# Kernel tuning notes

Hardware: AMD Instinct MI355X
Metric: run time of the kernel (lower is better)

The kernel has to match this reference:

```python
import jax, jax.numpy as jnp
import numpy as np

K, N, D, M, M_RF, N_RF = 512, 512, 16, 64, 16, 64


def cmul(a, b):
    # complex matmul with stacked real/imag in axis -3: a [...,2,m,k], b [...,2,k,n]
    ar, ai = a[..., 0, :, :], a[..., 1, :, :]
    br, bi = b[..., 0, :, :], b[..., 1, :, :]
    return jnp.stack([ar @ br - ai @ bi, ar @ bi + ai @ br], axis=-3)


def conjT(a):
    # complex conjugate transpose
    ar, ai = a[..., 0, :, :], a[..., 1, :, :]
    return jnp.stack([jnp.swapaxes(ar, -1, -2), -jnp.swapaxes(ai, -1, -2)], axis=-3)


def cinv(a):
    # inverse of complex matrix a=[2,n,n] via real 2n x 2n block matrix
    ar, ai = a[0], a[1]
    n = ar.shape[0]
    Mblk = jnp.block([[ar, -ai], [ai, ar]])
    Minv = jnp.linalg.inv(Mblk)
    return jnp.stack([Minv[:n, :n], Minv[n:, :n]], axis=0)


def setup_inputs() -> dict:
    key = jax.random.key(0)
    ks = jax.random.split(key, 8)
    s = 0.05  # keep accumulated products well-scaled
    H = s * jax.random.normal(ks[0], (K, 2, M, N), jnp.float32)
    U_RF = s * jax.random.normal(ks[1], (K, 2, M, M_RF), jnp.float32)
    U_BB = s * jax.random.normal(ks[2], (K, 2, M_RF, D), jnp.float32)
    W = s * jax.random.normal(ks[3], (K, 2, D, D), jnp.float32)
    V_RF = s * jax.random.normal(ks[4], (2, N, N_RF), jnp.float32)
    V_BB = s * jax.random.normal(ks[5], (K, 2, N_RF, D), jnp.float32)
    Y = s * jax.random.normal(ks[6], (K, 2, N, D), jnp.float32)
    rho = jnp.ones((1,), jnp.float32)  # forward arg, unused by the module
    rho_X_layer = jnp.asarray(6.0, jnp.float32)  # learned scalar
    mu = jnp.asarray(1.0, jnp.float32)           # learned scalar
    params4 = 0.001 * jax.random.normal(ks[7], (K, 2, N, D), jnp.float32)
    return dict(H=H, U_RF=U_RF, U_BB=U_BB, W=W, V_RF=V_RF, V_BB=V_BB, Y=Y,
                rho=rho, rho_X_layer=rho_X_layer, mu=mu, params4=params4)


def reference(H, U_RF, U_BB, W, V_RF, V_BB, Y, rho, rho_X_layer, mu, params4):
    # temp[k] = H[k]^H U_RF[k] U_BB[k] : [K,2,N,d]
    temp = cmul(cmul(conjT(H), U_RF), U_BB)
    TW = cmul(temp, W)  # [K,2,N,d]
    # A_rho = sum_k temp W temp^H + I/(2 rho) : [2,N,N]
    A_rho = cmul(TW, conjT(temp)).sum(axis=0)
    I = jnp.stack([jnp.eye(N, dtype=H.dtype), jnp.zeros((N, N), H.dtype)], axis=0)
    A_rho = A_rho + (1.0 / (2.0 * rho_X_layer)) * I
    # B_rho[k] = temp W + 0.5*(V_RF V_BB[k]/rho - Y[k]) : [K,2,N,d]
    B_rho = TW + 0.5 * ((1.0 / rho_X_layer) * cmul(V_RF, V_BB) - Y)
    A_inv = cinv(A_rho + mu * I)  # [2,N,N]
    X = cmul(A_inv, B_rho) + params4  # [K,2,N,d]
    return X
```

## Files before the change

kernel.cpp:

```cpp
#include <hip/hip_runtime.h>

#define KK 512
#define NN 512
#define DD 16
#define MM 64
#define MRF 16
#define NRF 64

typedef __attribute__((ext_vector_type(8))) short bf16x8;
typedef __attribute__((ext_vector_type(4))) float f32x4;
typedef __attribute__((ext_vector_type(8))) unsigned short u16x8;
typedef __attribute__((ext_vector_type(4))) unsigned short u16x4;

#define MFMA16 __builtin_amdgcn_mfma_f32_16x16x32_bf16

static __device__ __forceinline__ unsigned short f2bf(float x) {
    unsigned int u = __float_as_uint(x);
    u += 0x7fffu + ((u >> 16) & 1u);
    return (unsigned short)(u >> 16);
}
static __device__ __forceinline__ float bf2f(unsigned short b) {
    return __uint_as_float((unsigned int)b << 16);
}

__global__ __launch_bounds__(256) void vrfb_kernel(
    const float* __restrict__ V_RF, unsigned short* __restrict__ VRFb)
{
    const int idx = blockIdx.x*256 + threadIdx.x;
    const int n = idx >> 7, j = idx & 127;
    const int p = j >> 6, r = j & 63;
    VRFb[idx] = f2bf(V_RF[((size_t)p*NN + n)*NRF + r]);
}

__global__ __launch_bounds__(256) void small_kernel(
    const float* __restrict__ U_RF, const float* __restrict__ U_BB,
    const float* __restrict__ W, const float* __restrict__ V_BB,
    unsigned short* __restrict__ GT2, unsigned short* __restrict__ VBT2)
{
    const int k = blockIdx.x, t = threadIdx.x;
    __shared__ float sUR[2][MM][17];
    __shared__ float sUB[2][MRF][DD], sW[2][DD][DD];
    __shared__ float sVB[2][NRF][17];
    __shared__ float sG[2][MM][17], sGW[2][MM][17];

    const float* uf = U_RF + (size_t)k*2*MM*MRF;
    for (int i = t; i < 2*MM*MRF; i += 256) sUR[i>>10][(i>>4)&63][i&15] = uf[i];
    const float* ub = U_BB + (size_t)k*2*MRF*DD;
    for (int i = t; i < 2*MRF*DD; i += 256) sUB[i>>8][(i>>4)&15][i&15] = ub[i];
    const float* ww = W + (size_t)k*2*DD*DD;
    for (int i = t; i < 2*DD*DD; i += 256) sW[i>>8][(i>>4)&15][i&15] = ww[i];
    const float* vb = V_BB + (size_t)k*2*NRF*DD;
    for (int i = t; i < 2*NRF*DD; i += 256) sVB[i>>10][(i>>4)&63][i&15] = vb[i];
    __syncthreads();

    {
        const int m = t >> 2, dq = (t & 3) * 4;
        float gr[4] = {0,0,0,0}, gi[4] = {0,0,0,0};
#pragma unroll
        for (int r = 0; r < MRF; ++r) {
            const float ur = sUR[0][m][r], ui = sUR[1][m][r];
#pragma unroll
            for (int q = 0; q < 4; ++q) {
                const float br = sUB[0][r][dq+q], bi = sUB[1][r][dq+q];
                gr[q] += ur*br - ui*bi;
                gi[q] += ur*bi + ui*br;
            }
        }
#pragma unroll
        for (int q = 0; q < 4; ++q) { sG[0][m][dq+q] = gr[q]; sG[1][m][dq+q] = gi[q]; }
    }
    __syncthreads();

    {
        const int m = t >> 2, dq = (t & 3) * 4;
        float gwr[4] = {0,0,0,0}, gwi[4] = {0,0,0,0};
#pragma unroll
        for (int dp = 0; dp < DD; ++dp) {
            const float gr = sG[0][m][dp], gi = sG[1][m][dp];
#pragma unroll
            for (int q = 0; q < 4; ++q) {
                const float wr = sW[0][dp][dq+q], wi = sW[1][dp][dq+q];
                gwr[q] += gr*wr - gi*wi;
                gwi[q] += gr*wi + gi*wr;
            }
        }
#pragma unroll
        for (int q = 0; q < 4; ++q) { sGW[0][m][dq+q] = gwr[q]; sGW[1][m][dq+q] = gwi[q]; }
    }
    __syncthreads();

    {
        const int row = t >> 2, cq = t & 3;
        const int s = row >> 4, d = row & 15;
        const float (*P)[MM][17] = (s < 2) ? sG : sGW;
        const int im = s & 1;
        unsigned short* dst = GT2 + (((size_t)k*4 + s)*DD + d)*128;
#pragma unroll
        for (int cb = 0; cb < 4; ++cb) {
            u16x8 pk;
#pragma unroll
            for (int q = 0; q < 8; ++q) {
                const int c = cb*32 + cq*8 + q;
                const int m = c & 63, hi = c >> 6;
                float v;
                if (!im) v = hi ? P[1][m][d] : P[0][m][d];
                else     v = hi ? -P[0][m][d] : P[1][m][d];
                pk[q] = f2bf(v);
            }
            *reinterpret_cast<u16x8*>(dst + cb*32 + cq*8) = pk;
        }
    }
    {
        const int row = t >> 3, cq = t & 7;
        const int s = row >> 4, d = row & 15;
        unsigned short* dst = VBT2 + (((size_t)k*2 + s)*DD + d)*128;
#pragma unroll
        for (int cb = 0; cb < 2; ++cb) {
            u16x8 pk;
#pragma unroll
            for (int q = 0; q < 8; ++q) {
                const int c = cb*64 + cq*8 + q;
                const int r = c & 63, hi = c >> 6;
                float v;
                if (s == 0) v = hi ? -sVB[1][r][d] : sVB[0][r][d];
                else        v = hi ?  sVB[0][r][d] : sVB[1][r][d];
                pk[q] = f2bf(v);
            }
            *reinterpret_cast<u16x8*>(dst + cb*64 + cq*8) = pk;
        }
    }
}

__global__ __launch_bounds__(256) void prep_main(
    const float* __restrict__ H, const unsigned short* __restrict__ GT2,
    const unsigned short* __restrict__ VBT2, const unsigned short* __restrict__ VRFb,
    const float* __restrict__ Y, const float* __restrict__ rhoX,
    unsigned short* __restrict__ tempb, unsigned short* __restrict__ TWb,
    unsigned short* __restrict__ Bb)
{
    const int k  = blockIdx.x;
    const int nq = blockIdx.y;
    const int w = threadIdx.x >> 6, lane = threadIdx.x & 63;
    const int c = lane & 15, kg = lane >> 4;
    const float irx = 1.f / rhoX[0];

    const int nA = nq*128 + w*32 + c;
    const int nB = nA + 16;
    const float* Hk = H + (size_t)k*128*NN;

    f32x4 acc[12];
#pragma unroll
    for (int q = 0; q < 12; ++q) acc[q] = (f32x4)0.f;

#pragma unroll
    for (int ks = 0; ks < 4; ++ks) {
        const int slot0 = ks*32 + kg*8;
        const unsigned short* gbase = GT2 + ((size_t)k*4*DD + c)*128 + slot0;
        const bf16x8 g0 = *reinterpret_cast<const bf16x8*>(gbase);
        const bf16x8 g1 = *reinterpret_cast<const bf16x8*>(gbase + (size_t)DD*128);
        const bf16x8 g2 = *reinterpret_cast<const bf16x8*>(gbase + (size_t)2*DD*128);
        const bf16x8 g3 = *reinterpret_cast<const bf16x8*>(gbase + (size_t)3*DD*128);
        const unsigned short* vbase = VBT2 + ((size_t)k*2*DD + c)*128 + slot0;
        const bf16x8 v0 = *reinterpret_cast<const bf16x8*>(vbase);
        const bf16x8 v1 = *reinterpret_cast<const bf16x8*>(vbase + (size_t)DD*128);

        float hA[8], hB[8];
#pragma unroll
        for (int e = 0; e < 8; ++e) {
            hA[e] = Hk[(size_t)(slot0 + e)*NN + nA];
            hB[e] = Hk[(size_t)(slot0 + e)*NN + nB];
        }
        const bf16x8 bvA = *reinterpret_cast<const bf16x8*>(VRFb + (size_t)nA*128 + slot0);
        const bf16x8 bvB = *reinterpret_cast<const bf16x8*>(VRFb + (size_t)nB*128 + slot0);
        bf16x8 bhA, bhB;
#pragma unroll
        for (int e = 0; e < 8; ++e) {
            bhA[e] = (short)f2bf(hA[e]);
            bhB[e] = (short)f2bf(hB[e]);
        }
        acc[0]  = MFMA16(g0, bhA, acc[0],  0,0,0);
        acc[1]  = MFMA16(g0, bhB, acc[1],  0,0,0);
        acc[2]  = MFMA16(g1, bhA, acc[2],  0,0,0);
        acc[3]  = MFMA16(g1, bhB, acc[3],  0,0,0);
        acc[4]  = MFMA16(g2, bhA, acc[4],  0,0,0);
        acc[5]  = MFMA16(g2, bhB, acc[5],  0,0,0);
        acc[6]  = MFMA16(g3, bhA, acc[6],  0,0,0);
        acc[7]  = MFMA16(g3, bhB, acc[7],  0,0,0);
        acc[8]  = MFMA16(v0, bvA, acc[8],  0,0,0);
        acc[9]  = MFMA16(v0, bvB, acc[9],  0,0,0);
        acc[10] = MFMA16(v1, bvA, acc[10], 0,0,0);
        acc[11] = MFMA16(v1, bvB, acc[11], 0,0,0);
    }

#pragma unroll
    for (int t = 0; t < 2; ++t) {
        const int n = t ? nB : nA;
        const size_t o0 = ((size_t)(k*2 + 0)*NN + n)*DD + kg*4;
        const size_t o1 = ((size_t)(k*2 + 1)*NN + n)*DD + kg*4;
        const float4 y0 = *reinterpret_cast<const float4*>(Y + o0);
        const float4 y1 = *reinterpret_cast<const float4*>(Y + o1);
        const float y0a[4] = {y0.x, y0.y, y0.z, y0.w};
        const float y1a[4] = {y1.x, y1.y, y1.z, y1.w};
        u16x4 tr_, ti_, wr_, wi_, br_, bi_;
#pragma unroll
        for (int r = 0; r < 4; ++r) {
            tr_[r] = f2bf(acc[0+t][r]);  ti_[r] = f2bf(acc[2+t][r]);
            wr_[r] = f2bf(acc[4+t][r]);  wi_[r] = f2bf(acc[6+t][r]);
            br_[r] = f2bf(acc[4+t][r] + 0.5f*(acc[8+t][r]*irx  - y0a[r]));
            bi_[r] = f2bf(acc[6+t][r] + 0.5f*(acc[10+t][r]*irx - y1a[r]));
        }
        *reinterpret_cast<u16x4*>(tempb + o0) = tr_;
        *reinterpret_cast<u16x4*>(tempb + o1) = ti_;
        *reinterpret_cast<u16x4*>(TWb + o0)   = wr_;
        *reinterpret_cast<u16x4*>(TWb + o1)   = wi_;
        *reinterpret_cast<u16x4*>(Bb + o0)    = br_;
        *reinterpret_cast<u16x4*>(Bb + o1)    = bi_;
    }
}

__global__ __launch_bounds__(256) void egemm_kernel(
    const unsigned short* __restrict__ TWb, const unsigned short* __restrict__ tmpb,
    float* __restrict__ Epart)
{
    const int ib = blockIdx.x >> 3;
    const int ks = blockIdx.x & 7;
    const int jb = blockIdx.y;
    const int w    = threadIdx.x >> 6;
    const int lane = threadIdx.x & 63;
    const int m  = lane & 15;
    const int kg = lane >> 4;
    const int iw = ib*64 + (w>>1)*32;
    const int jw = jb*64 + (w&1)*32;
    const int d0  = (kg & 1) * 8;
    const int kof = kg >> 1;

    f32x4 RR[2][2], II[2][2], RI[2][2], IR[2][2];
#pragma unroll
    for (int is = 0; is < 2; ++is)
#pragma unroll
        for (int js = 0; js < 2; ++js) {
            RR[is][js] = (f32x4)0.f; II[is][js] = (f32x4)0.f;
            RI[is][js] = (f32x4)0.f; IR[is][js] = (f32x4)0.f;
        }

#pragma unroll 2
    for (int c = 0; c < 32; ++c) {
        const int chunk = ks*32 + c;
        const int kp = chunk*2 + kof;
        const unsigned short* Ab = TWb  + ((size_t)(kp*2+0)*NN + iw + m)*DD + d0;
        const unsigned short* Bb2 = tmpb + ((size_t)(kp*2+0)*NN + jw + m)*DD + d0;
        bf16x8 ar[2], ai[2], br[2], bi[2];
#pragma unroll
        for (int is = 0; is < 2; ++is) {
            ar[is] = *reinterpret_cast<const bf16x8*>(Ab + (size_t)is*16*DD);
            ai[is] = *reinterpret_cast<const bf16x8*>(Ab + (size_t)NN*DD + (size_t)is*16*DD);
        }
#pragma unroll
        for (int js = 0; js < 2; ++js) {
            br[js] = *reinterpret_cast<const bf16x8*>(Bb2 + (size_t)js*16*DD);
            bi[js] = *reinterpret_cast<const bf16x8*>(Bb2 + (size_t)NN*DD + (size_t)js*16*DD);
        }
#pragma unroll
        for (int is = 0; is < 2; ++is)
#pragma unroll
            for (int js = 0; js < 2; ++js) {
                RR[is][js] = MFMA16(ar[is], br[js], RR[is][js], 0, 0, 0);
                II[is][js] = MFMA16(ai[is], bi[js], II[is][js], 0, 0, 0);
                RI[is][js] = MFMA16(ar[is], bi[js], RI[is][js], 0, 0, 0);
                IR[is][js] = MFMA16(ai[is], br[js], IR[is][js], 0, 0, 0);
            }
    }

    float* Eb = Epart + (size_t)ks*2*NN*NN;
#pragma unroll
    for (int is = 0; is < 2; ++is)
#pragma unroll
        for (int js = 0; js < 2; ++js) {
            const int i = iw + is*16 + kg*4;
            const int jx = jw + js*16 + m;
#pragma unroll
            for (int r = 0; r < 4; ++r) {
                Eb[(size_t)(i+r)*NN + jx]               = RR[is][js][r] + II[is][js][r];
                Eb[(size_t)NN*NN + (size_t)(i+r)*NN + jx] = IR[is][js][r] - RI[is][js][r];
            }
        }
}

__global__ __launch_bounds__(256) void reduceinit_kernel(
    const float* __restrict__ Epart,
    const float* __restrict__ rhoX, const float* __restrict__ mu,
    unsigned short* __restrict__ P, unsigned short* __restrict__ PT,
    unsigned short* __restrict__ T1, unsigned short* __restrict__ T1T)
{
    const size_t idx = (size_t)blockIdx.x*256 + threadIdx.x;
    const float ic = 1.f / (1.f/(2.f*rhoX[0]) + mu[0]);
    const size_t pl = (size_t)2*NN*NN;
    float s = 0.f;
#pragma unroll
    for (int ks = 0; ks < 8; ++ks) s += Epart[(size_t)ks*pl + idx];
    const float mm = s * ic;
    const int p = (int)(idx / ((size_t)NN*NN));
    const size_t rem = idx - (size_t)p*NN*NN;
    const int i = (int)(rem / NN), jx = (int)(rem % NN);
    const unsigned short pv = f2bf(-mm);
    const unsigned short tv = f2bf(((p == 0 && i == jx) ? 1.f : 0.f) - mm);
    const size_t tidx = (size_t)p*NN*NN + (size_t)jx*NN + i;
    P[idx] = pv;  PT[tidx] = pv;
    T1[idx] = tv; T1T[tidx] = tv;
}

template<bool ADD_B, bool WRITE_T>
__global__ __launch_bounds__(256) void mm_kernel(
    const unsigned short* __restrict__ A, const unsigned short* __restrict__ BT,
    unsigned short* __restrict__ D, unsigned short* __restrict__ DT)
{
    const int w    = threadIdx.x >> 6;
    const int lane = threadIdx.x & 63;
    const int m  = lane & 15;
    const int kg = lane >> 4;
    const int i0 = blockIdx.y*32;
    const int j0 = blockIdx.x*32;
    const int iw = (w>>1)*16;
    const int jw = (w&1)*16;

    __shared__ unsigned short sD[2][32][34];

    f32x4 RR = (f32x4)0.f, II = (f32x4)0.f, RI = (f32x4)0.f, IR = (f32x4)0.f;

#pragma unroll 4
    for (int c = 0; c < 16; ++c) {
        const int l0 = c*32 + kg*8;
        const bf16x8 ar = *reinterpret_cast<const bf16x8*>(A  + (size_t)(i0+iw+m)*NN + l0);
        const bf16x8 ai = *reinterpret_cast<const bf16x8*>(A  + (size_t)NN*NN + (size_t)(i0+iw+m)*NN + l0);
        const bf16x8 br = *reinterpret_cast<const bf16x8*>(BT + (size_t)(j0+jw+m)*NN + l0);
        const bf16x8 bi = *reinterpret_cast<const bf16x8*>(BT + (size_t)NN*NN + (size_t)(j0+jw+m)*NN + l0);
        RR = MFMA16(ar, br, RR, 0, 0, 0);
        II = MFMA16(ai, bi, II, 0, 0, 0);
        RI = MFMA16(ar, bi, RI, 0, 0, 0);
        IR = MFMA16(ai, br, IR, 0, 0, 0);
    }
    const int i = i0 + iw + kg*4;
    const int jx = j0 + jw + m;
    float adr[4] = {0.f,0.f,0.f,0.f}, adi[4] = {0.f,0.f,0.f,0.f};
    if (ADD_B) {
        const u16x4 badr = *reinterpret_cast<const u16x4*>(BT + (size_t)jx*NN + i);
        const u16x4 badi = *reinterpret_cast<const u16x4*>(BT + (size_t)NN*NN + (size_t)jx*NN + i);
#pragma unroll
        for (int r = 0; r < 4; ++r) { adr[r] = bf2f(badr[r]); adi[r] = bf2f(badi[r]); }
    }
#pragma unroll
    for (int r = 0; r < 4; ++r) {
        const unsigned short dr_ = f2bf(RR[r] - II[r] + adr[r]);
        const unsigned short di_ = f2bf(RI[r] + IR[r] + adi[r]);
        D[(size_t)(i+r)*NN + jx] = dr_;
        D[(size_t)NN*NN + (size_t)(i+r)*NN + jx] = di_;
        if (WRITE_T) {
            sD[0][iw + kg*4 + r][jw + m] = dr_;
            sD[1][iw + kg*4 + r][jw + m] = di_;
        }
    }
    if (WRITE_T) {
        __syncthreads();
        const int t = threadIdx.x;
        const int r8 = t >> 2, seg = t & 3;
        const int plane = r8 >> 5, jloc = r8 & 31;
        u16x8 v;
#pragma unroll
        for (int e = 0; e < 8; ++e) v[e] = sD[plane][seg*8 + e][jloc];
        *reinterpret_cast<u16x8*>(DT + (size_t)plane*NN*NN +
                                  (size_t)(j0 + jloc)*NN + i0 + seg*8) = v;
    }
}

__global__ __launch_bounds__(256) void final_kernel(
    const unsigned short* __restrict__ Sb, const unsigned short* __restrict__ Bb,
    const float* __restrict__ par4,
    const float* __restrict__ rhoX, const float* __restrict__ mu,
    float* __restrict__ Xout)
{
    const int k0 = blockIdx.x * 2;
    __shared__ __align__(16) unsigned short sBT[2][2][DD][520];

#pragma unroll
    for (int kk = 0; kk < 2; ++kk) {
        const unsigned short* Bk = Bb + (size_t)(k0 + kk)*2*NN*DD;
        for (int q = 0; q < 8; ++q) {
            const int t8 = q*256 + threadIdx.x;
            const u16x8 v = *reinterpret_cast<const u16x8*>(Bk + (size_t)t8*8);
            const int flat = t8*8;
            const int p = flat >> 13, n = (flat >> 4) & 511, dd0 = flat & 15;
#pragma unroll
            for (int jj = 0; jj < 8; ++jj) sBT[kk][p][dd0+jj][n] = v[jj];
        }
    }
    __syncthreads();

    const int w    = threadIdx.x >> 6;
    const int lane = threadIdx.x & 63;
    const int m  = lane & 15;
    const int kg = lane >> 4;
    const int i0 = blockIdx.y*64 + w*16;

    f32x4 RR[2], II[2], RI[2], IR[2];
#pragma unroll
    for (int kk = 0; kk < 2; ++kk) {
        RR[kk] = (f32x4)0.f; II[kk] = (f32x4)0.f;
        RI[kk] = (f32x4)0.f; IR[kk] = (f32x4)0.f;
    }

#pragma unroll 2
    for (int c = 0; c < 16; ++c) {
        const int l0 = c*32 + kg*8;
        const bf16x8 ar = *reinterpret_cast<const bf16x8*>(Sb + (size_t)(i0+m)*NN + l0);
        const bf16x8 ai = *reinterpret_cast<const bf16x8*>(Sb + (size_t)NN*NN + (size_t)(i0+m)*NN + l0);
#pragma unroll
        for (int kk = 0; kk < 2; ++kk) {
            const bf16x8 br = *reinterpret_cast<const bf16x8*>(&sBT[kk][0][m][l0]);
            const bf16x8 bi = *reinterpret_cast<const bf16x8*>(&sBT[kk][1][m][l0]);
            RR[kk] = MFMA16(ar, br, RR[kk], 0, 0, 0);
            II[kk] = MFMA16(ai, bi, II[kk], 0, 0, 0);
            RI[kk] = MFMA16(ar, bi, RI[kk], 0, 0, 0);
            IR[kk] = MFMA16(ai, br, IR[kk], 0, 0, 0);
        }
    }
    const float ic = 1.f / (1.f/(2.f*rhoX[0]) + mu[0]);
#pragma unroll
    for (int kk = 0; kk < 2; ++kk) {
        const int k = k0 + kk;
#pragma unroll
        for (int r = 0; r < 4; ++r) {
            const int i = i0 + kg*4 + r;
            const int d = m;
            const size_t idx0 = ((size_t)(k*2+0)*NN + i)*DD + d;
            const size_t idx1 = ((size_t)(k*2+1)*NN + i)*DD + d;
            Xout[idx0] = (RR[kk][r] - II[kk][r])*ic + par4[idx0];
            Xout[idx1] = (RI[kk][r] + IR[kk][r])*ic + par4[idx1];
        }
    }
}

extern "C" void kernel_launch(void* const* d_in, const int* in_sizes, int n_in,
                              void* d_out, int out_size, void* d_ws, size_t ws_size,
                              hipStream_t stream) {
    const float* H     = (const float*)d_in[0];
    const float* U_RF  = (const float*)d_in[1];
    const float* U_BB  = (const float*)d_in[2];
    const float* W     = (const float*)d_in[3];
    const float* V_RF  = (const float*)d_in[4];
    const float* V_BB  = (const float*)d_in[5];
    const float* Y     = (const float*)d_in[6];
    const float* rhoX  = (const float*)d_in[8];
    const float* mu    = (const float*)d_in[9];
    const float* par4  = (const float*)d_in[10];
    float* Xout = (float*)d_out;

    unsigned short* u = (unsigned short*)d_ws;
    const size_t bigE = (size_t)KK*2*NN*DD;
    const size_t plE  = (size_t)2*NN*NN;
    unsigned short* tempb = u;
    unsigned short* TWb   = tempb + bigE;
    unsigned short* Bb    = TWb + bigE;
    unsigned short* GT2   = Bb + bigE;
    unsigned short* VBT2  = GT2 + (size_t)KK*4*DD*128;
    unsigned short* VRFb  = VBT2 + (size_t)KK*2*DD*128;
    unsigned short* Pm    = VRFb + (size_t)NN*128;
    unsigned short* PmT   = Pm  + plE;
    unsigned short* T1    = PmT + plE;
    unsigned short* T1T   = T1  + plE;
    unsigned short* Q     = T1T + plE;
    unsigned short* QT    = Q   + plE;
    unsigned short* R     = QT  + plE;
    unsigned short* RT    = R   + plE;
    unsigned short* T2    = RT  + plE;
    unsigned short* T2T   = T2  + plE;
    unsigned short* T3    = T2T + plE;
    unsigned short* T3T   = T3  + plE;
    unsigned short* R2    = T3T + plE;
    unsigned short* Ss    = R2  + plE;
    float* Epart = (float*)(Ss + plE);

    vrfb_kernel<<<256, 256, 0, stream>>>(V_RF, VRFb);
    small_kernel<<<KK, 256, 0, stream>>>(U_RF, U_BB, W, V_BB, GT2, VBT2);
    prep_main<<<dim3(KK, 4), 256, 0, stream>>>(H, GT2, VBT2, VRFb, Y, rhoX,
                                               tempb, TWb, Bb);
    egemm_kernel<<<dim3(64, 8), 256, 0, stream>>>(TWb, tempb, Epart);
    reduceinit_kernel<<<(int)(plE/256), 256, 0, stream>>>(Epart, rhoX, mu,
                                                          Pm, PmT, T1, T1T);
    mm_kernel<false,true ><<<dim3(16,16), 256, 0, stream>>>(Pm, PmT, Q,  QT);
    mm_kernel<true ,true ><<<dim3(16,16), 256, 0, stream>>>(Q,  T1T, T2, T2T);
    mm_kernel<false,true ><<<dim3(16,16), 256, 0, stream>>>(Q,  QT,  R,  RT);
    mm_kernel<true ,true ><<<dim3(16,16), 256, 0, stream>>>(R,  T2T, T3, T3T);
    mm_kernel<false,false><<<dim3(16,16), 256, 0, stream>>>(R,  RT,  R2, nullptr);
    mm_kernel<true ,false><<<dim3(16,16), 256, 0, stream>>>(R2, T3T, Ss, nullptr);
    final_kernel<<<dim3(KK/2, 8), 256, 0, stream>>>(Ss, Bb, par4, rhoX, mu, Xout);
}
```

Baseline: 228.9 us.

## Stage H tiles through LDS with coalesced float4 loads in prep_main

prep_main now loads each block's 128x64 slice of H with coalesced float4 reads, converts it to packed bf16 pairs and stores it in shared memory. Each wave then reads its MFMA B-fragments from LDS instead of issuing strided scalar global loads. Each block covers 64 columns instead of 128, so the grid doubles and each wave holds 6 accumulators instead of 12. Separately, the mm_kernel inner loop unroll goes from 4 to 8. The cost is an LDS round trip and a barrier per block, and the GT2/VBT2 fragment loads are repeated across twice as many blocks.

```diff
diff --git a/kernel.cpp b/kernel.cpp
--- a/kernel.cpp
+++ b/kernel.cpp
@@ -22,6 +22,8 @@
 static __device__ __forceinline__ float bf2f(unsigned short b) {
     return __uint_as_float((unsigned int)b << 16);
 }
+
+union frag_cast { uint4 u; bf16x8 v; };
 
 __global__ __launch_bounds__(256) void vrfb_kernel(
     const float* __restrict__ V_RF, unsigned short* __restrict__ VRFb)
@@ -139,22 +141,50 @@
     unsigned short* __restrict__ Bb)
 {
     const int k  = blockIdx.x;
-    const int nq = blockIdx.y;
-    const int w = threadIdx.x >> 6, lane = threadIdx.x & 63;
+    const int nb = blockIdx.y;
+    const int t  = threadIdx.x;
+    const int n0 = nb*64;
+
+    __shared__ unsigned int sH[64][65];
+
+    const float* Hk = H + (size_t)k*128*NN + n0;
+#pragma unroll
+    for (int pass = 0; pass < 4; ++pass) {
+        const int e2 = pass*16 + (t >> 4);
+        const int c4 = (t & 15) * 4;
+        const float4 a = *reinterpret_cast<const float4*>(Hk + (size_t)(2*e2  )*NN + c4);
+        const float4 b = *reinterpret_cast<const float4*>(Hk + (size_t)(2*e2+1)*NN + c4);
+        uint4 d;
+        d.x = (unsigned int)f2bf(a.x) | ((unsigned int)f2bf(b.x) << 16);
+        d.y = (unsigned int)f2bf(a.y) | ((unsigned int)f2bf(b.y) << 16);
+        d.z = (unsigned int)f2bf(a.z) | ((unsigned int)f2bf(b.z) << 16);
+        d.w = (unsigned int)f2bf(a.w) | ((unsigned int)f2bf(b.w) << 16);
+        *reinterpret_cast<uint4*>(&sH[e2][c4]) = d;
+    }
+    __syncthreads();
+
+    const int w = t >> 6, lane = t & 63;
     const int c = lane & 15, kg = lane >> 4;
     const float irx = 1.f / rhoX[0];
-
-    const int nA = nq*128 + w*32 + c;
-    const int nB = nA + 16;
-    const float* Hk = H + (size_t)k*128*NN;
-
-    f32x4 acc[12];
-#pragma unroll
-    for (int q = 0; q < 12; ++q) acc[q] = (f32x4)0.f;
+    const int ncol = w*16 + c;
+    const int n = n0 + ncol;
+
+    f32x4 aTr = (f32x4)0.f, aTi = (f32x4)0.f;
+    f32x4 aWr = (f32x4)0.f, aWi = (f32x4)0.f;
+    f32x4 aVr = (f32x4)0.f, aVi = (f32x4)0.f;
 
 #pragma unroll
     for (int ks = 0; ks < 4; ++ks) {
         const int slot0 = ks*32 + kg*8;
+        const int e2b = ks*16 + kg*4;
+        frag_cast fc;
+        fc.u.x = sH[e2b+0][ncol];
+        fc.u.y = sH[e2b+1][ncol];
+        fc.u.z = sH[e2b+2][ncol];
+        fc.u.w = sH[e2b+3][ncol];
+        const bf16x8 bh = fc.v;
+        const bf16x8 bv = *reinterpret_cast<const bf16x8*>(VRFb + (size_t)n*128 + slot0);
+
         const unsigned short* gbase = GT2 + ((size_t)k*4*DD + c)*128 + slot0;
         const bf16x8 g0 = *reinterpret_cast<const bf16x8*>(gbase);
         const bf16x8 g1 = *reinterpret_cast<const bf16x8*>(gbase + (size_t)DD*128);
@@ -164,37 +194,15 @@
         const bf16x8 v0 = *reinterpret_cast<const bf16x8*>(vbase);
         const bf16x8 v1 = *reinterpret_cast<const bf16x8*>(vbase + (size_t)DD*128);
 
-        float hA[8], hB[8];
-#pragma unroll
-        for (int e = 0; e < 8; ++e) {
-            hA[e] = Hk[(size_t)(slot0 + e)*NN + nA];
-            hB[e] = Hk[(size_t)(slot0 + e)*NN + nB];
-        }
-        const bf16x8 bvA = *reinterpret_cast<const bf16x8*>(VRFb + (size_t)nA*128 + slot0);
-        const bf16x8 bvB = *reinterpret_cast<const bf16x8*>(VRFb + (size_t)nB*128 + slot0);
-        bf16x8 bhA, bhB;
-#pragma unroll
-        for (int e = 0; e < 8; ++e) {
-            bhA[e] = (short)f2bf(hA[e]);
-            bhB[e] = (short)f2bf(hB[e]);
-        }
-        acc[0]  = MFMA16(g0, bhA, acc[0],  0,0,0);
-        acc[1]  = MFMA16(g0, bhB, acc[1],  0,0,0);
-        acc[2]  = MFMA16(g1, bhA, acc[2],  0,0,0);
-        acc[3]  = MFMA16(g1, bhB, acc[3],  0,0,0);
-        acc[4]  = MFMA16(g2, bhA, acc[4],  0,0,0);
-        acc[5]  = MFMA16(g2, bhB, acc[5],  0,0,0);
-        acc[6]  = MFMA16(g3, bhA, acc[6],  0,0,0);
-        acc[7]  = MFMA16(g3, bhB, acc[7],  0,0,0);
-        acc[8]  = MFMA16(v0, bvA, acc[8],  0,0,0);
-        acc[9]  = MFMA16(v0, bvB, acc[9],  0,0,0);
-        acc[10] = MFMA16(v1, bvA, acc[10], 0,0,0);
-        acc[11] = MFMA16(v1, bvB, acc[11], 0,0,0);
-    }
-
-#pragma unroll
-    for (int t = 0; t < 2; ++t) {
-        const int n = t ? nB : nA;
+        aTr = MFMA16(g0, bh, aTr, 0, 0, 0);
+        aTi = MFMA16(g1, bh, aTi, 0, 0, 0);
+        aWr = MFMA16(g2, bh, aWr, 0, 0, 0);
+        aWi = MFMA16(g3, bh, aWi, 0, 0, 0);
+        aVr = MFMA16(v0, bv, aVr, 0, 0, 0);
+        aVi = MFMA16(v1, bv, aVi, 0, 0, 0);
+    }
+
+    {
         const size_t o0 = ((size_t)(k*2 + 0)*NN + n)*DD + kg*4;
         const size_t o1 = ((size_t)(k*2 + 1)*NN + n)*DD + kg*4;
         const float4 y0 = *reinterpret_cast<const float4*>(Y + o0);
@@ -204,10 +212,10 @@
         u16x4 tr_, ti_, wr_, wi_, br_, bi_;
 #pragma unroll
         for (int r = 0; r < 4; ++r) {
-            tr_[r] = f2bf(acc[0+t][r]);  ti_[r] = f2bf(acc[2+t][r]);
-            wr_[r] = f2bf(acc[4+t][r]);  wi_[r] = f2bf(acc[6+t][r]);
-            br_[r] = f2bf(acc[4+t][r] + 0.5f*(acc[8+t][r]*irx  - y0a[r]));
-            bi_[r] = f2bf(acc[6+t][r] + 0.5f*(acc[10+t][r]*irx - y1a[r]));
+            tr_[r] = f2bf(aTr[r]);  ti_[r] = f2bf(aTi[r]);
+            wr_[r] = f2bf(aWr[r]);  wi_[r] = f2bf(aWi[r]);
+            br_[r] = f2bf(aWr[r] + 0.5f*(aVr[r]*irx - y0a[r]));
+            bi_[r] = f2bf(aWi[r] + 0.5f*(aVi[r]*irx - y1a[r]));
         }
         *reinterpret_cast<u16x4*>(tempb + o0) = tr_;
         *reinterpret_cast<u16x4*>(tempb + o1) = ti_;
@@ -327,7 +335,7 @@
 
     f32x4 RR = (f32x4)0.f, II = (f32x4)0.f, RI = (f32x4)0.f, IR = (f32x4)0.f;
 
-#pragma unroll 4
+#pragma unroll 8
     for (int c = 0; c < 16; ++c) {
         const int l0 = c*32 + kg*8;
         const bf16x8 ar = *reinterpret_cast<const bf16x8*>(A  + (size_t)(i0+iw+m)*NN + l0);
@@ -481,7 +489,7 @@
 
     vrfb_kernel<<<256, 256, 0, stream>>>(V_RF, VRFb);
     small_kernel<<<KK, 256, 0, stream>>>(U_RF, U_BB, W, V_BB, GT2, VBT2);
-    prep_main<<<dim3(KK, 4), 256, 0, stream>>>(H, GT2, VBT2, VRFb, Y, rhoX,
+    prep_main<<<dim3(KK, 8), 256, 0, stream>>>(H, GT2, VBT2, VRFb, Y, rhoX,
                                                tempb, TWb, Bb);
     egemm_kernel<<<dim3(64, 8), 256, 0, stream>>>(TWb, tempb, Epart);
     reduceinit_kernel<<<(int)(plE/256), 256, 0, stream>>>(Epart, rhoX, mu,
```

Measured after the change: 241.1 us. +5.3%, slower.
